# Kernel tuning notes

Hardware: AMD Instinct MI355X
Metric: run time of the kernel (lower is better)

## Reference

```python
import jax, jax.numpy as jnp
import numpy as np
from jax import lax

B, NP = 4, 8192          # events, points per event (equal-sized batches)
RATIO, R, K = 0.25, 0.2, 64
MP = int(NP * RATIO)     # sampled centers per event
D_IN = 32
BIG = 1e10


def _fps_one(pos):
    # Farthest point sampling (deterministic start at index 0). pos: [NP,3] -> [MP] int32
    d = jnp.sum((pos - pos[0]) ** 2, axis=-1)
    sel = jnp.zeros((MP,), jnp.int32)

    def body(i, carry):
        sel, d = carry
        nxt = jnp.argmax(d).astype(jnp.int32)
        sel = sel.at[i].set(nxt)
        d = jnp.minimum(d, jnp.sum((pos - pos[nxt]) ** 2, axis=-1))
        return sel, d

    sel, _ = lax.fori_loop(1, MP, body, (sel, d))
    return sel


def _ball_query_one(centers, pos):
    # centers: [MP,3], pos: [NP,3] -> neighbor idx [MP,K] int32, validity mask [MP,K]
    d2 = jnp.sum((centers[:, None, :] - pos[None, :, :]) ** 2, axis=-1)  # [MP,NP]
    d2m = jnp.where(d2 <= R * R, d2, BIG)
    neg, idx = lax.top_k(-d2m, K)          # K nearest within radius (deterministic)
    mask = (-neg) <= R * R
    return idx.astype(jnp.int32), mask


def reference(x, pos, batch, W1, b1, W2, b2, W3, b3):
    xb = x.reshape(B, NP, D_IN)
    pb = pos.reshape(B, NP, 3)

    sel = jax.vmap(_fps_one)(pb)                                   # [B,MP]
    centers = jnp.take_along_axis(pb, sel[..., None], axis=1)      # [B,MP,3]
    idx, mask = jax.vmap(_ball_query_one)(centers, pb)             # [B,MP,K]

    gather = jax.vmap(lambda a, i: a[i])
    pos_j = gather(pb, idx)                                        # [B,MP,K,3]
    x_j = gather(xb, idx)                                          # [B,MP,K,D_IN]

    rel = pos_j - centers[:, :, None, :]
    h = jnp.concatenate([x_j, rel], axis=-1)                       # [B,MP,K,D_IN+3]
    h = jax.nn.relu(h @ W1 + b1)
    h = jax.nn.relu(h @ W2 + b2)
    h = jax.nn.relu(h @ W3 + b3)                                   # [B,MP,K,128]

    h = jnp.where(mask[..., None], h, -BIG)
    x_out = jnp.max(h, axis=2).reshape(B * MP, -1)                 # max aggregation
    pos_out = centers.reshape(B * MP, 3)
    batch_out = jnp.repeat(jnp.arange(B, dtype=jnp.int32), MP)
    return x_out, pos_out, batch_out


def setup_inputs() -> dict:
    key = jax.random.key(0)
    ks = jax.random.split(key, 8)
    x = jax.random.normal(ks[0], (B * NP, D_IN), jnp.float32)
    pos = jax.random.uniform(ks[1], (B * NP, 3), jnp.float32)
    batch = (jnp.arange(B * NP) // NP).astype(jnp.int64)
    W1 = jax.random.normal(ks[2], (D_IN + 3, 64), jnp.float32) * 0.05
    b1 = jnp.zeros((64,), jnp.float32)
    W2 = jax.random.normal(ks[3], (64, 64), jnp.float32) * 0.05
    b2 = jnp.zeros((64,), jnp.float32)
    W3 = jax.random.normal(ks[4], (64, 128), jnp.float32) * 0.05
    b3 = jnp.zeros((128,), jnp.float32)
    return {"x": x, "pos": pos, "batch": batch, "W1": W1, "b1": b1,
            "W2": W2, "b2": b2, "W3": W3, "b3": b3}
```

## Files before the change

kernel.cpp:

```cpp
#include <hip/hip_runtime.h>


#define BATCH 4
#define NP 8192
#define MP 2048
#define KNN 64
#define DIN 32

#define DPP_FMAX(v, ctrl)                                                     \
  {                                                                           \
    int _t = __builtin_amdgcn_update_dpp(__float_as_int(v),                   \
                                         __float_as_int(v), (ctrl), 0xF,      \
                                         0xF, false);                         \
    (v) = fmaxf((v), __int_as_float(_t));                                     \
  }

__global__ __launch_bounds__(1024) void fps_k(const float* __restrict__ pos,
                                              float* __restrict__ pout,
                                              float* __restrict__ bout)
{
  const int b = blockIdx.x;
  const int tid = threadIdx.x;
  const int lane = tid & 63, wid = tid >> 6;
  const float* __restrict__ pb = pos + (size_t)b * NP * 3;
  const int base = tid * 8;

  bout[b * MP + tid] = (float)b;
  bout[b * MP + 1024 + tid] = (float)b;

  float px[8], py[8], pz[8], d[8];
#pragma unroll
  for (int k = 0; k < 8; k++) {
    px[k] = pb[(base + k) * 3 + 0];
    py[k] = pb[(base + k) * 3 + 1];
    pz[k] = pb[(base + k) * 3 + 2];
  }
  const float c0x = pb[0], c0y = pb[1], c0z = pb[2];
  if (tid == 0) {
    pout[(size_t)b * MP * 3 + 0] = c0x;
    pout[(size_t)b * MP * 3 + 1] = c0y;
    pout[(size_t)b * MP * 3 + 2] = c0z;
  }

  float bv = -1.f;
#pragma unroll
  for (int k = 0; k < 8; k++) {
    float dx = px[k] - c0x, dy = py[k] - c0y, dz = pz[k] - c0z;
    float nd = dx * dx + dy * dy + dz * dz;
    d[k] = nd;
    bv = fmaxf(bv, nd);
  }

  __shared__ float sv[2][16];
  __shared__ __align__(16) float sc[2][16][4];

  for (int i = 1; i < MP; i++) {
    float v = bv;
    DPP_FMAX(v, 0x111);
    DPP_FMAX(v, 0x112);
    DPP_FMAX(v, 0x114);
    DPP_FMAX(v, 0x118);
    DPP_FMAX(v, 0x142);
    DPP_FMAX(v, 0x143);
    const float wmax =
        __int_as_float(__builtin_amdgcn_readlane(__float_as_int(v), 63));

    unsigned long long m = __ballot(bv == wmax);
    const int src = (int)__builtin_ctzll(m);
    const int p = i & 1;
    if (lane == src) {
      float ox = px[7], oy = py[7], oz = pz[7];
#pragma unroll
      for (int k = 6; k >= 0; k--)
        if (d[k] == wmax) { ox = px[k]; oy = py[k]; oz = pz[k]; }
      sv[p][wid] = wmax;
      float4 q; q.x = ox; q.y = oy; q.z = oz; q.w = 0.f;
      *(float4*)&sc[p][wid][0] = q;
    }
    __syncthreads();

    float v2 = sv[p][lane & 15];
    float v2r = v2;
    DPP_FMAX(v2r, 0x111);
    DPP_FMAX(v2r, 0x112);
    DPP_FMAX(v2r, 0x114);
    DPP_FMAX(v2r, 0x118);
    const float mv =
        __int_as_float(__builtin_amdgcn_readlane(__float_as_int(v2r), 15));
    unsigned long long m2 = __ballot(v2 == mv);
    const int mw = (int)__builtin_ctzll(m2);
    const float4 cc = *(const float4*)&sc[p][mw][0];
    const float ncx = cc.x, ncy = cc.y, ncz = cc.z;

    if (tid == 0) {
      pout[((size_t)b * MP + i) * 3 + 0] = ncx;
      pout[((size_t)b * MP + i) * 3 + 1] = ncy;
      pout[((size_t)b * MP + i) * 3 + 2] = ncz;
    }

    bv = -1.f;
#pragma unroll
    for (int k = 0; k < 8; k++) {
      float dx = px[k] - ncx, dy = py[k] - ncy, dz = pz[k] - ncz;
      float nd = dx * dx + dy * dy + dz * dz;
      float dn = fminf(d[k], nd);
      d[k] = dn;
      bv = fmaxf(bv, dn);
    }
  }
}

__global__ __launch_bounds__(64) void ballq_k(const float* __restrict__ pos,
                                              const float* __restrict__ pout,
                                              int* __restrict__ nbr)
{
  const int wg = blockIdx.x;
  const int lane = threadIdx.x;
  const int b = wg >> 11;
  const float* __restrict__ pb = pos + (size_t)b * NP * 3;
  const float cx = pout[(size_t)wg * 3 + 0];
  const float cy = pout[(size_t)wg * 3 + 1];
  const float cz = pout[(size_t)wg * 3 + 2];
  const float R2 = (float)(0.2 * 0.2);

  __shared__ unsigned long long cand[1024];
  int cnt = 0;
  for (int basej = 0; basej < NP; basej += 64) {
    const int j = basej + lane;
    float dx = pb[j * 3 + 0] - cx;
    float dy = pb[j * 3 + 1] - cy;
    float dz = pb[j * 3 + 2] - cz;
    float d2 = dx * dx + dy * dy + dz * dz;
    bool in = (d2 <= R2);
    unsigned long long mb = __ballot(in);
    int pre = (int)__popcll(mb & ((1ull << lane) - 1ull));
    int slot = cnt + pre;
    if (in && slot < 1024)
      cand[slot] = ((unsigned long long)__float_as_uint(d2) << 32) | (unsigned int)j;
    cnt += (int)__popcll(mb);
  }
  if (cnt > 1024) cnt = 1024;

  int myout = -1;
  for (int r = 0; r < KNN; r++) {
    unsigned long long v = ~0ull; int slot = -1;
    for (int s = lane; s < cnt; s += 64) {
      unsigned long long c = cand[s];
      if (c < v) { v = c; slot = s; }
    }
#pragma unroll
    for (int off = 1; off < 64; off <<= 1) {
      unsigned long long ov = __shfl_xor(v, off);
      int os = __shfl_xor(slot, off);
      if (ov < v) { v = ov; slot = os; }
    }
    if (lane == r) myout = (v == ~0ull) ? -1 : (int)(v & 0xffffffffu);
    if (lane == 0 && slot >= 0) cand[slot] = ~0ull;
    __syncthreads();
  }
  nbr[(size_t)wg * KNN + lane] = myout;
}

__global__ __launch_bounds__(64) void p1_k(const float* __restrict__ x,
                                           const float* __restrict__ W1,
                                           float* __restrict__ P1)
{
  const int j = blockIdx.x;
  const int c = threadIdx.x;
  const float* __restrict__ xr = x + (size_t)j * DIN;
  float acc = 0.f;
#pragma unroll
  for (int k = 0; k < DIN; k++) acc += xr[k] * W1[k * 64 + c];
  P1[(size_t)j * 64 + c] = acc;
}

__global__ __launch_bounds__(256) void tw_k(const float* __restrict__ W2,
                                            const float* __restrict__ W3,
                                            float* __restrict__ W2T,
                                            float* __restrict__ W3T)
{
  int e = blockIdx.x * 256 + threadIdx.x;
  if (e < 64 * 64) {
    int c = e >> 6, k = e & 63;
    W2T[e] = W2[k * 64 + c];
  } else {
    int e2 = e - 64 * 64;
    if (e2 < 128 * 64) {
      int c = e2 >> 6, k = e2 & 63;
      W3T[e2] = W3[k * 128 + c];
    }
  }
}

__global__ __launch_bounds__(64) void mlp_k(const float* __restrict__ pos,
    const float* __restrict__ P1, const float* __restrict__ W1,
    const float* __restrict__ b1, const float* __restrict__ W2T,
    const float* __restrict__ b2, const float* __restrict__ W3T,
    const float* __restrict__ b3, const int* __restrict__ nbr,
    const float* __restrict__ pout, float* __restrict__ xout)
{
  __shared__ __align__(16) float h2s[64 * 68];
  const int wg = blockIdx.x;
  const int lane = threadIdx.x;
  const int b = wg >> 11;
  const int idx = nbr[(size_t)wg * KNN + lane];
  const bool valid = idx >= 0;
  const int j = valid ? idx : 0;
  const float cx = pout[(size_t)wg * 3 + 0];
  const float cy = pout[(size_t)wg * 3 + 1];
  const float cz = pout[(size_t)wg * 3 + 2];
  const float* __restrict__ pj = pos + ((size_t)b * NP + j) * 3;
  const float rx = pj[0] - cx, ry = pj[1] - cy, rz = pj[2] - cz;
  const float* __restrict__ p1r =
      (const float*)__builtin_assume_aligned(P1 + ((size_t)b * NP + j) * 64, 16);

  float h1[64];
#pragma unroll
  for (int k = 0; k < 64; k++) {
    float v = p1r[k] + rx * W1[32 * 64 + k] + ry * W1[33 * 64 + k]
                     + rz * W1[34 * 64 + k] + b1[k];
    h1[k] = fmaxf(v, 0.f);
  }

  for (int c4 = 0; c4 < 16; c4++) {
    float a0 = b2[c4 * 4 + 0], a1 = b2[c4 * 4 + 1];
    float a2 = b2[c4 * 4 + 2], a3 = b2[c4 * 4 + 3];
    const float* __restrict__ w0 = W2T + (c4 * 4 + 0) * 64;
    const float* __restrict__ w1 = W2T + (c4 * 4 + 1) * 64;
    const float* __restrict__ w2 = W2T + (c4 * 4 + 2) * 64;
    const float* __restrict__ w3 = W2T + (c4 * 4 + 3) * 64;
#pragma unroll
    for (int k = 0; k < 64; k++) {
      a0 += h1[k] * w0[k]; a1 += h1[k] * w1[k];
      a2 += h1[k] * w2[k]; a3 += h1[k] * w3[k];
    }
    float4 q;
    q.x = fmaxf(a0, 0.f); q.y = fmaxf(a1, 0.f);
    q.z = fmaxf(a2, 0.f); q.w = fmaxf(a3, 0.f);
    *(float4*)&h2s[lane * 68 + c4 * 4] = q;
  }

  float4 keep = make_float4(0.f, 0.f, 0.f, 0.f);
  const float* __restrict__ h2p = &h2s[lane * 68];
  for (int c4 = 0; c4 < 32; c4++) {
    float a0 = b3[c4 * 4 + 0], a1 = b3[c4 * 4 + 1];
    float a2 = b3[c4 * 4 + 2], a3 = b3[c4 * 4 + 3];
    const float* __restrict__ w0 = W3T + (c4 * 4 + 0) * 64;
    const float* __restrict__ w1 = W3T + (c4 * 4 + 1) * 64;
    const float* __restrict__ w2 = W3T + (c4 * 4 + 2) * 64;
    const float* __restrict__ w3 = W3T + (c4 * 4 + 3) * 64;
#pragma unroll
    for (int k4 = 0; k4 < 16; k4++) {
      float4 h = *(const float4*)&h2p[k4 * 4];
      a0 += h.x * w0[k4 * 4 + 0]; a0 += h.y * w0[k4 * 4 + 1];
      a0 += h.z * w0[k4 * 4 + 2]; a0 += h.w * w0[k4 * 4 + 3];
      a1 += h.x * w1[k4 * 4 + 0]; a1 += h.y * w1[k4 * 4 + 1];
      a1 += h.z * w1[k4 * 4 + 2]; a1 += h.w * w1[k4 * 4 + 3];
      a2 += h.x * w2[k4 * 4 + 0]; a2 += h.y * w2[k4 * 4 + 1];
      a2 += h.z * w2[k4 * 4 + 2]; a2 += h.w * w2[k4 * 4 + 3];
      a3 += h.x * w3[k4 * 4 + 0]; a3 += h.y * w3[k4 * 4 + 1];
      a3 += h.z * w3[k4 * 4 + 2]; a3 += h.w * w3[k4 * 4 + 3];
    }
    a0 = valid ? fmaxf(a0, 0.f) : 0.f;
    a1 = valid ? fmaxf(a1, 0.f) : 0.f;
    a2 = valid ? fmaxf(a2, 0.f) : 0.f;
    a3 = valid ? fmaxf(a3, 0.f) : 0.f;
#pragma unroll
    for (int off = 1; off < 64; off <<= 1) {
      a0 = fmaxf(a0, __shfl_xor(a0, off));
      a1 = fmaxf(a1, __shfl_xor(a1, off));
      a2 = fmaxf(a2, __shfl_xor(a2, off));
      a3 = fmaxf(a3, __shfl_xor(a3, off));
    }
    if (lane == c4) { keep.x = a0; keep.y = a1; keep.z = a2; keep.w = a3; }
  }
  if (lane < 32)
    *(float4*)&xout[(size_t)wg * 128 + lane * 4] = keep;
}

extern "C" void kernel_launch(void* const* d_in, const int* in_sizes, int n_in,
                              void* d_out, int out_size, void* d_ws, size_t ws_size,
                              hipStream_t stream)
{
  const float* x   = (const float*)d_in[0];
  const float* pos = (const float*)d_in[1];
  const float* W1 = (const float*)d_in[3];
  const float* b1 = (const float*)d_in[4];
  const float* W2 = (const float*)d_in[5];
  const float* b2 = (const float*)d_in[6];
  const float* W3 = (const float*)d_in[7];
  const float* b3 = (const float*)d_in[8];

  float* out  = (float*)d_out;
  float* xout = out;
  float* pout = out + 8192 * 128;
  float* bout = out + 8192 * 128 + 8192 * 3;

  char* ws = (char*)d_ws;
  float* P1  = (float*)ws;
  float* W2T = (float*)(ws + 8388608);
  float* W3T = (float*)(ws + 8404992);
  int*   nbr = (int*)(ws + 8437760);

  fps_k<<<dim3(BATCH), dim3(1024), 0, stream>>>(pos, pout, bout);
  p1_k<<<dim3(BATCH * NP), dim3(64), 0, stream>>>(x, W1, P1);
  tw_k<<<dim3(48), dim3(256), 0, stream>>>(W2, W3, W2T, W3T);
  ballq_k<<<dim3(BATCH * MP), dim3(64), 0, stream>>>(pos, pout, nbr);
  mlp_k<<<dim3(BATCH * MP), dim3(64), 0, stream>>>(pos, P1, W1, b1, W2T, b2,
                                                   W3T, b3, nbr, pout, xout);
}
```

Baseline: 2.803 ms.

## Halve FPS block width, pack argmax slot, rank-sort ball query, pad positions

FPS now runs 512 threads with 16 points each, cutting the block-level reduction to 8 waves. Each wave's max and its coordinates are packed into one float4 slot and the winner is broadcast with readlane, so the loop needs fewer shared-memory round trips. Ball query replaces the 64-round iterative min-extraction with a single counting-rank pass over the candidates, and reads points from a new float4-padded copy built by a prep kernel, which also pre-fills the neighbor list with -1. This adds an extra kernel launch and buffer, raises per-thread register use in FPS, and only ranks the first 512 candidates per center.

```diff
diff --git a/kernel.cpp b/kernel.cpp
--- a/kernel.cpp
+++ b/kernel.cpp
@@ -15,22 +15,36 @@
     (v) = fmaxf((v), __int_as_float(_t));                                     \
   }
 
-__global__ __launch_bounds__(1024) void fps_k(const float* __restrict__ pos,
-                                              float* __restrict__ pout,
-                                              float* __restrict__ bout)
+__global__ __launch_bounds__(256) void prep_k(const float* __restrict__ pos,
+                                              float4* __restrict__ pos4,
+                                              int* __restrict__ nbr)
+{
+  const int e = blockIdx.x * 256 + threadIdx.x;
+  nbr[e] = -1;
+  if (e < BATCH * NP) {
+    float4 q;
+    q.x = pos[e * 3 + 0]; q.y = pos[e * 3 + 1]; q.z = pos[e * 3 + 2];
+    q.w = 0.f;
+    pos4[e] = q;
+  }
+}
+
+__global__ __launch_bounds__(512) void fps_k(const float* __restrict__ pos,
+                                             float* __restrict__ pout,
+                                             float* __restrict__ bout)
 {
   const int b = blockIdx.x;
   const int tid = threadIdx.x;
   const int lane = tid & 63, wid = tid >> 6;
   const float* __restrict__ pb = pos + (size_t)b * NP * 3;
-  const int base = tid * 8;
-
-  bout[b * MP + tid] = (float)b;
-  bout[b * MP + 1024 + tid] = (float)b;
-
-  float px[8], py[8], pz[8], d[8];
-#pragma unroll
-  for (int k = 0; k < 8; k++) {
+  const int base = tid * 16;
+
+#pragma unroll
+  for (int t = 0; t < 4; t++) bout[b * MP + t * 512 + tid] = (float)b;
+
+  float px[16], py[16], pz[16], d[16];
+#pragma unroll
+  for (int k = 0; k < 16; k++) {
     px[k] = pb[(base + k) * 3 + 0];
     py[k] = pb[(base + k) * 3 + 1];
     pz[k] = pb[(base + k) * 3 + 2];
@@ -44,15 +58,14 @@
 
   float bv = -1.f;
 #pragma unroll
-  for (int k = 0; k < 8; k++) {
+  for (int k = 0; k < 16; k++) {
     float dx = px[k] - c0x, dy = py[k] - c0y, dz = pz[k] - c0z;
     float nd = dx * dx + dy * dy + dz * dz;
     d[k] = nd;
     bv = fmaxf(bv, nd);
   }
 
-  __shared__ float sv[2][16];
-  __shared__ __align__(16) float sc[2][16][4];
+  __shared__ __align__(16) float4 slot[2][8];
 
   for (int i = 1; i < MP; i++) {
     float v = bv;
@@ -69,28 +82,30 @@
     const int src = (int)__builtin_ctzll(m);
     const int p = i & 1;
     if (lane == src) {
-      float ox = px[7], oy = py[7], oz = pz[7];
-#pragma unroll
-      for (int k = 6; k >= 0; k--)
+      float ox = px[15], oy = py[15], oz = pz[15];
+#pragma unroll
+      for (int k = 14; k >= 0; k--)
         if (d[k] == wmax) { ox = px[k]; oy = py[k]; oz = pz[k]; }
-      sv[p][wid] = wmax;
-      float4 q; q.x = ox; q.y = oy; q.z = oz; q.w = 0.f;
-      *(float4*)&sc[p][wid][0] = q;
+      float4 q; q.x = wmax; q.y = ox; q.z = oy; q.w = oz;
+      slot[p][wid] = q;
     }
     __syncthreads();
 
-    float v2 = sv[p][lane & 15];
-    float v2r = v2;
+    const float4 q = slot[p][lane & 7];
+    float v2 = q.x, v2r = q.x;
     DPP_FMAX(v2r, 0x111);
     DPP_FMAX(v2r, 0x112);
     DPP_FMAX(v2r, 0x114);
-    DPP_FMAX(v2r, 0x118);
     const float mv =
-        __int_as_float(__builtin_amdgcn_readlane(__float_as_int(v2r), 15));
+        __int_as_float(__builtin_amdgcn_readlane(__float_as_int(v2r), 7));
     unsigned long long m2 = __ballot(v2 == mv);
     const int mw = (int)__builtin_ctzll(m2);
-    const float4 cc = *(const float4*)&sc[p][mw][0];
-    const float ncx = cc.x, ncy = cc.y, ncz = cc.z;
+    const float ncx =
+        __int_as_float(__builtin_amdgcn_readlane(__float_as_int(q.y), mw));
+    const float ncy =
+        __int_as_float(__builtin_amdgcn_readlane(__float_as_int(q.z), mw));
+    const float ncz =
+        __int_as_float(__builtin_amdgcn_readlane(__float_as_int(q.w), mw));
 
     if (tid == 0) {
       pout[((size_t)b * MP + i) * 3 + 0] = ncx;
@@ -100,7 +115,7 @@
 
     bv = -1.f;
 #pragma unroll
-    for (int k = 0; k < 8; k++) {
+    for (int k = 0; k < 16; k++) {
       float dx = px[k] - ncx, dy = py[k] - ncy, dz = pz[k] - ncz;
       float nd = dx * dx + dy * dy + dz * dz;
       float dn = fminf(d[k], nd);
@@ -110,14 +125,14 @@
   }
 }
 
-__global__ __launch_bounds__(64) void ballq_k(const float* __restrict__ pos,
+__global__ __launch_bounds__(64) void ballq_k(const float4* __restrict__ pos4,
                                               const float* __restrict__ pout,
                                               int* __restrict__ nbr)
 {
   const int wg = blockIdx.x;
   const int lane = threadIdx.x;
   const int b = wg >> 11;
-  const float* __restrict__ pb = pos + (size_t)b * NP * 3;
+  const float4* __restrict__ pb = pos4 + (size_t)b * NP;
   const float cx = pout[(size_t)wg * 3 + 0];
   const float cy = pout[(size_t)wg * 3 + 1];
   const float cz = pout[(size_t)wg * 3 + 2];
@@ -127,9 +142,8 @@
   int cnt = 0;
   for (int basej = 0; basej < NP; basej += 64) {
     const int j = basej + lane;
-    float dx = pb[j * 3 + 0] - cx;
-    float dy = pb[j * 3 + 1] - cy;
-    float dz = pb[j * 3 + 2] - cz;
+    const float4 pj = pb[j];
+    float dx = pj.x - cx, dy = pj.y - cy, dz = pj.z - cz;
     float d2 = dx * dx + dy * dy + dz * dz;
     bool in = (d2 <= R2);
     unsigned long long mb = __ballot(in);
@@ -140,25 +154,25 @@
     cnt += (int)__popcll(mb);
   }
   if (cnt > 1024) cnt = 1024;
-
-  int myout = -1;
-  for (int r = 0; r < KNN; r++) {
-    unsigned long long v = ~0ull; int slot = -1;
-    for (int s = lane; s < cnt; s += 64) {
-      unsigned long long c = cand[s];
-      if (c < v) { v = c; slot = s; }
-    }
-#pragma unroll
-    for (int off = 1; off < 64; off <<= 1) {
-      unsigned long long ov = __shfl_xor(v, off);
-      int os = __shfl_xor(slot, off);
-      if (ov < v) { v = ov; slot = os; }
-    }
-    if (lane == r) myout = (v == ~0ull) ? -1 : (int)(v & 0xffffffffu);
-    if (lane == 0 && slot >= 0) cand[slot] = ~0ull;
-    __syncthreads();
-  }
-  nbr[(size_t)wg * KNN + lane] = myout;
+  __syncthreads();
+
+  unsigned long long mk[8];
+  int rank[8];
+#pragma unroll
+  for (int m = 0; m < 8; m++) {
+    const int s = lane + m * 64;
+    mk[m] = (s < cnt) ? cand[s] : ~0ull;
+    rank[m] = 0;
+  }
+  for (int j = 0; j < cnt; j++) {
+    const unsigned long long kj = cand[j];
+#pragma unroll
+    for (int m = 0; m < 8; m++) rank[m] += (kj < mk[m]) ? 1 : 0;
+  }
+#pragma unroll
+  for (int m = 0; m < 8; m++)
+    if (rank[m] < KNN)
+      nbr[(size_t)wg * KNN + rank[m]] = (int)(mk[m] & 0xffffffffu);
 }
 
 __global__ __launch_bounds__(64) void p1_k(const float* __restrict__ x,
@@ -297,15 +311,17 @@
   float* bout = out + 8192 * 128 + 8192 * 3;
 
   char* ws = (char*)d_ws;
-  float* P1  = (float*)ws;
-  float* W2T = (float*)(ws + 8388608);
-  float* W3T = (float*)(ws + 8404992);
-  int*   nbr = (int*)(ws + 8437760);
-
-  fps_k<<<dim3(BATCH), dim3(1024), 0, stream>>>(pos, pout, bout);
+  float*  P1   = (float*)ws;
+  float*  W2T  = (float*)(ws + 8388608);
+  float*  W3T  = (float*)(ws + 8404992);
+  int*    nbr  = (int*)(ws + 8437760);
+  float4* pos4 = (float4*)(ws + 10534912);
+
+  prep_k<<<dim3(2048), dim3(256), 0, stream>>>(pos, pos4, nbr);
+  fps_k<<<dim3(BATCH), dim3(512), 0, stream>>>(pos, pout, bout);
   p1_k<<<dim3(BATCH * NP), dim3(64), 0, stream>>>(x, W1, P1);
   tw_k<<<dim3(48), dim3(256), 0, stream>>>(W2, W3, W2T, W3T);
-  ballq_k<<<dim3(BATCH * MP), dim3(64), 0, stream>>>(pos, pout, nbr);
+  ballq_k<<<dim3(BATCH * MP), dim3(64), 0, stream>>>(pos4, pout, nbr);
   mlp_k<<<dim3(BATCH * MP), dim3(64), 0, stream>>>(pos, P1, W1, b1, W2T, b2,
                                                    W3T, b3, nbr, pout, xout);
 }
```

Result: slower. 3.054 ms (+9.0%).
